# Kernel optimization log

Hardware: AMD Instinct MI355X
Metric: run time of the kernel (lower is better)

Reference implementation:

```python
import jax, jax.numpy as jnp
import numpy as np

VOCAB, EMB, H, LAYERS, B, T = 50000, 128, 128, 3, 64, 512


def _lstm_dir(x, w_ih, w_hh, b_ih, b_hh, h0, c0, reverse):
    # x: [B,T,Din]; w_ih: [4H,Din]; w_hh: [4H,H]; h0,c0: [B,H]
    xg = jnp.einsum('btd,gd->btg', x, w_ih) + b_ih + b_hh  # [B,T,4H]

    def step(carry, xg_t):
        h, c = carry
        g = xg_t + h @ w_hh.T  # [B,4H]
        i, f, gg, o = jnp.split(g, 4, axis=-1)  # torch gate order i,f,g,o
        c = jax.nn.sigmoid(f) * c + jax.nn.sigmoid(i) * jnp.tanh(gg)
        h = jax.nn.sigmoid(o) * jnp.tanh(c)
        return (h, c), h

    _, hs = jax.lax.scan(step, (h0, c0), jnp.swapaxes(xg, 0, 1), reverse=reverse)
    return jnp.swapaxes(hs, 0, 1)  # [B,T,H], aligned with input time order


def _bidir_layer(x, w_ih, w_hh, b_ih, b_hh, h0, c0):
    # stacked params: leading dim 2 = (fwd, bwd)
    fwd = _lstm_dir(x, w_ih[0], w_hh[0], b_ih[0], b_hh[0], h0[0], c0[0], False)
    bwd = _lstm_dir(x, w_ih[1], w_hh[1], b_ih[1], b_hh[1], h0[1], c0[1], True)
    return jnp.concatenate([fwd, bwd], axis=-1)  # [B,T,2H]


def setup_inputs() -> dict:
    key = jax.random.key(0)
    ks = jax.random.split(key, 20)
    s = 1.0 / np.sqrt(H)
    inp = {
        'X_batch': jax.random.randint(ks[0], (B, T), 0, VOCAB),
        'emb': jax.random.normal(ks[1], (VOCAB, EMB), jnp.float32),
        'hx': jax.random.normal(ks[2], (2 * LAYERS, B, H), jnp.float32),
        'cx': jax.random.normal(ks[3], (2 * LAYERS, B, H), jnp.float32),
        'lin_w': jax.random.uniform(ks[4], (1, 2 * H), jnp.float32, -s, s),
        'lin_b': jax.random.uniform(ks[5], (1,), jnp.float32, -s, s),
    }
    k = 6
    for l in range(LAYERS):
        din = EMB if l == 0 else 2 * H
        inp[f'w_ih_{l}'] = jax.random.uniform(ks[k], (2, 4 * H, din), jnp.float32, -s, s); k += 1
        inp[f'w_hh_{l}'] = jax.random.uniform(ks[k], (2, 4 * H, H), jnp.float32, -s, s); k += 1
        inp[f'b_ih_{l}'] = jax.random.uniform(ks[k], (2, 4 * H), jnp.float32, -s, s); k += 1
        inp[f'b_hh_{l}'] = jax.random.uniform(ks[k], (2, 4 * H), jnp.float32, -s, s); k += 1
    return inp


def reference(X_batch, emb, hx, cx, lin_w, lin_b,
              w_ih_0, w_hh_0, b_ih_0, b_hh_0,
              w_ih_1, w_hh_1, b_ih_1, b_hh_1,
              w_ih_2, w_hh_2, b_ih_2, b_hh_2):
    x = emb[X_batch]  # [B,T,EMB]
    params = [(w_ih_0, w_hh_0, b_ih_0, b_hh_0),
              (w_ih_1, w_hh_1, b_ih_1, b_hh_1),
              (w_ih_2, w_hh_2, b_ih_2, b_hh_2)]
    for l, (wi, wh, bi, bh) in enumerate(params):
        x = _bidir_layer(x, wi, wh, bi, bh, hx[2 * l:2 * l + 2], cx[2 * l:2 * l + 2])
    # linear head applied to last timestep (== output[:, -1] of full linear)
    return x[:, -1] @ lin_w.T + lin_b  # [B,1]
```

## Files before the change

### kernel.cpp

```cpp
#include <hip/hip_runtime.h>
#include <hip/hip_bf16.h>
#include <stdint.h>

#define B_    64
#define T_    512
#define EMB_  128
#define H_    128
#define G4    512
#define M_    (B_ * T_)

typedef __attribute__((ext_vector_type(8))) short     short8;
typedef __attribute__((ext_vector_type(4))) float     floatx4;
typedef __attribute__((ext_vector_type(2))) _Float16  half2v;

#define GLDS(g, l) __builtin_amdgcn_global_load_lds( \
    (__attribute__((address_space(1))) void*)(g),    \
    (__attribute__((address_space(3))) void*)(l), 16, 0, 0)

__device__ __forceinline__ unsigned short f2bf_bits(float f) {
  __hip_bfloat16 h = __float2bfloat16(f);
  return *reinterpret_cast<unsigned short*>(&h);
}
__device__ __forceinline__ float bf_bits2f(unsigned short u) {
  unsigned int x = ((unsigned int)u) << 16;
  return __uint_as_float(x);
}
__device__ __forceinline__ float sigm(float x) {
  return __fdividef(1.0f, 1.0f + __expf(-x));
}
__device__ __forceinline__ float tanh_fast(float x) {
  return 1.0f - __fdividef(2.0f, __expf(2.0f * x) + 1.0f);
}

__device__ __forceinline__ unsigned int pack_f16x2(float a, float b) {
  half2v h; h.x = (_Float16)a; h.y = (_Float16)b;
  return __builtin_bit_cast(unsigned int, h);
}
__device__ __forceinline__ half2v u2h2(unsigned int u) {
  return __builtin_bit_cast(half2v, u);
}

#if __has_builtin(__builtin_amdgcn_fdot2)
__device__ __forceinline__ float fdot2(half2v a, half2v b, float c) {
  return __builtin_amdgcn_fdot2(a, b, c, false);
}
#else
__device__ __forceinline__ float fdot2(half2v a, half2v b, float c) {
  return fmaf((float)a.x, (float)b.x, fmaf((float)a.y, (float)b.y, c));
}
#endif

__device__ __forceinline__ float pair_bfly_add(float x) {
  return x + __int_as_float(
      __builtin_amdgcn_mov_dpp(__float_as_int(x), 0xB1, 0xF, 0xF, true));
}

__device__ __forceinline__ void barrier_lds_only() {
  __builtin_amdgcn_s_waitcnt(0xC07F);
  __builtin_amdgcn_s_barrier();
}

__device__ __forceinline__ void  store_xg(float* p, float v)  { *p = v; }
__device__ __forceinline__ void  store_xg(unsigned short* p, float v) { *p = f2bf_bits(v); }
__device__ __forceinline__ float load_xg(const float* p)  { return *p; }
__device__ __forceinline__ float load_xg(const unsigned short* p) { return bf_bits2f(*p); }

__global__ void k_gather(const int* __restrict__ X, const float* __restrict__ emb,
                         unsigned short* __restrict__ x0) {
  int i = blockIdx.x * 256 + threadIdx.x;
  int row = i >> 5, c4 = i & 31;
  float4 v = ((const float4*)emb)[(size_t)X[row] * 32 + c4];
  ushort4 o;
  o.x = f2bf_bits(v.x); o.y = f2bf_bits(v.y); o.z = f2bf_bits(v.z); o.w = f2bf_bits(v.w);
  ((ushort4*)x0)[i] = o;
}

__global__ void k_prep(const float* __restrict__ w, const float* __restrict__ bi,
                       const float* __restrict__ bh, unsigned short* __restrict__ wb,
                       float* __restrict__ bias, int nw) {
  int i = blockIdx.x * blockDim.x + threadIdx.x;
  int stride = gridDim.x * blockDim.x;
  for (int k = i; k < nw; k += stride) wb[k] = f2bf_bits(w[k]);
  for (int k = i; k < 2 * G4; k += stride) bias[k] = bi[k] + bh[k];
}

__global__ void k_prep_whh(const float* __restrict__ Whh, unsigned int* __restrict__ wf) {
  int i = blockIdx.x * 256 + threadIdx.x;
  int dir = i >> 15;
  int r   = i & 0x7FFF;
  int i4  = r >> 10;
  int r2  = r & 0x3FF;
  int ts  = r2 >> 2;
  int q   = r2 & 3;
  int d   = i4 * 4 + q;
  int g   = d >> 5;
  int jj  = d & 31;
  int lane = ts & 63, w = ts >> 6;
  int p = lane & 1, ul = lane >> 1;
  int u = w * 32 + ul;
  int k = 64 * p + 2 * jj;
  const float* wr = Whh + ((size_t)dir * G4 + g * H_ + u) * H_ + k;
  wf[i] = pack_f16x2(wr[0], wr[1]);
}

template <typename XG_T>
__global__ __launch_bounds__(256, 2) void k_gemm(
    const unsigned short* __restrict__ A,
    const unsigned short* __restrict__ W,
    const float* __restrict__ bias,
    XG_T* __restrict__ xg,
    int K) {
  __shared__ unsigned short sA[128 * 32];
  __shared__ unsigned short sB[128 * 32];
  const int tid  = threadIdx.x;
  const int lane = tid & 63;
  const int wave = tid >> 6;
  const int mt = blockIdx.x, nt = blockIdx.y, dir = blockIdx.z;
  const size_t Arow0 = (size_t)mt * 128;
  const int    Ncol0 = nt * 128;
  const unsigned short* Wd = W + (size_t)dir * G4 * K;

  const int srow = tid >> 2;
  const int qlog = (tid & 3) ^ ((tid >> 4) & 3);
  auto ldsA0 = (__attribute__((address_space(3))) void*)(sA + wave * 512);
  auto ldsA1 = (__attribute__((address_space(3))) void*)(sA + 2048 + wave * 512);
  auto ldsB0 = (__attribute__((address_space(3))) void*)(sB + wave * 512);
  auto ldsB1 = (__attribute__((address_space(3))) void*)(sB + 2048 + wave * 512);

  floatx4 acc[4][4];
#pragma unroll
  for (int i = 0; i < 4; ++i)
#pragma unroll
    for (int j = 0; j < 4; ++j) acc[i][j] = (floatx4)0.0f;

  const int wrow = (wave >> 1) * 64, wcol = (wave & 1) * 64;
  const int frow = lane & 15;
  const int fq   = lane >> 4;

  for (int kt = 0; kt < K; kt += 32) {
    const unsigned short* gA0 = A  + (Arow0 + srow) * (size_t)K + kt + qlog * 8;
    const unsigned short* gB0 = Wd + (size_t)(Ncol0 + srow) * K + kt + qlog * 8;
    GLDS(gA0, ldsA0);
    GLDS(gA0 + (size_t)64 * K, ldsA1);
    GLDS(gB0, ldsB0);
    GLDS(gB0 + (size_t)64 * K, ldsB1);
    __syncthreads();

    short8 af[4], bf[4];
#pragma unroll
    for (int i = 0; i < 4; ++i) {
      int r  = wrow + 16 * i + frow;
      int rn = wcol + 16 * i + frow;
      af[i] = *(const short8*)(sA + r  * 32 + ((fq ^ ((r  >> 2) & 3)) * 8));
      bf[i] = *(const short8*)(sB + rn * 32 + ((fq ^ ((rn >> 2) & 3)) * 8));
    }
#pragma unroll
    for (int i = 0; i < 4; ++i)
#pragma unroll
      for (int j = 0; j < 4; ++j)
        acc[i][j] = __builtin_amdgcn_mfma_f32_16x16x32_bf16(af[i], bf[j], acc[i][j], 0, 0, 0);
    __syncthreads();
  }

  const int r0 = (lane >> 4) * 4;
  const int cc = lane & 15;
  XG_T* xgd = xg + (size_t)dir * M_ * G4;
#pragma unroll
  for (int j = 0; j < 4; ++j) {
    int gcol = Ncol0 + wcol + 16 * j + cc;
    float bs = bias[dir * G4 + gcol];
#pragma unroll
    for (int i = 0; i < 4; ++i) {
      size_t rowb = Arow0 + wrow + 16 * i + r0;
#pragma unroll
      for (int r = 0; r < 4; ++r)
        store_xg(&xgd[(rowb + r) * G4 + gcol], acc[i][j][r] + bs);
    }
  }
}

template <typename XG_T>
__global__ __attribute__((amdgpu_flat_work_group_size(256, 256),
                          amdgpu_waves_per_eu(1, 1))) void k_scan(
    const unsigned int* __restrict__ wf,
    const float* __restrict__ hx0,
    const float* __restrict__ cx0,
    const XG_T* __restrict__ xg,
    unsigned short* __restrict__ y)
{
  const int b   = blockIdx.x & 63;
  const int dir = blockIdx.x >> 6;
  const int tid = threadIdx.x;
  const int lane = tid & 63;
  const int wave = tid >> 6;
  const int p  = lane & 1;
  const int ul = lane >> 1;
  const int u  = wave * 32 + ul;

  __shared__ __align__(16) unsigned short h16[2][128];

  uint4 wv[32];
  const uint4* wfv = (const uint4*)wf;
#pragma unroll
  for (int i = 0; i < 32; ++i) wv[i] = wfv[(dir * 32 + i) * 256 + tid];

  float c = cx0[(size_t)dir * B_ * H_ + b * H_ + u];
  if (p == 0) {
    float h0 = hx0[(size_t)dir * B_ * H_ + b * H_ + u];
    h16[0][u] = (unsigned short)(pack_f16x2(h0, 0.0f) & 0xFFFF);
  }

  const XG_T* xgb = xg + ((size_t)dir * M_ + (size_t)b * T_) * G4;
  const intptr_t xstep = dir ? -(intptr_t)G4 : (intptr_t)G4;
  const int o0 = (2 * p) * H_ + u;
  const int o1 = o0 + H_;
  const XG_T* xrow0 = xgb + (dir ? (size_t)(T_ - 1) * G4 : 0);
  float xa0 = load_xg(xrow0 + o0), xb0 = load_xg(xrow0 + o1);
  float xa1 = load_xg(xrow0 + xstep + o0), xb1 = load_xg(xrow0 + xstep + o1);
  const XG_T* xld = xrow0 + 2 * xstep;

  unsigned short* yp = y + ((size_t)b * T_ + (dir ? T_ - 1 : 0)) * (2 * H_)
                         + dir * H_ + u;
  const intptr_t ystep = dir ? -(intptr_t)(2 * H_) : (intptr_t)(2 * H_);

  __syncthreads();

  auto dots = [&](int par, float xva, float xvb,
                  float& g0, float& g1, float& g2, float& g3) {
    const uint4* hv4 = (const uint4*)&h16[par][0];
    uint4 hq[8];
#pragma unroll
    for (int i = 0; i < 8; ++i) hq[i] = hv4[8 * p + i];
    half2v hh[32];
#pragma unroll
    for (int i = 0; i < 8; ++i) {
      hh[4 * i + 0] = u2h2(hq[i].x);
      hh[4 * i + 1] = u2h2(hq[i].y);
      hh[4 * i + 2] = u2h2(hq[i].z);
      hh[4 * i + 3] = u2h2(hq[i].w);
    }
    float A0 = 0, B0 = 0, A1 = 0, B1 = 0, A2 = 0, B2 = 0, A3 = 0, B3 = 0;
#pragma unroll
    for (int j = 0; j < 16; ++j) {
      int d0 = j, d1 = j + 16;
      A0 = fdot2(u2h2(((const unsigned int*)&wv[(0 * 32 + d0) >> 2])[(0 * 32 + d0) & 3]), hh[d0], A0);
      A1 = fdot2(u2h2(((const unsigned int*)&wv[(1 * 32 + d0) >> 2])[(1 * 32 + d0) & 3]), hh[d0], A1);
      A2 = fdot2(u2h2(((const unsigned int*)&wv[(2 * 32 + d0) >> 2])[(2 * 32 + d0) & 3]), hh[d0], A2);
      A3 = fdot2(u2h2(((const unsigned int*)&wv[(3 * 32 + d0) >> 2])[(3 * 32 + d0) & 3]), hh[d0], A3);
      B0 = fdot2(u2h2(((const unsigned int*)&wv[(0 * 32 + d1) >> 2])[(0 * 32 + d1) & 3]), hh[d1], B0);
      B1 = fdot2(u2h2(((const unsigned int*)&wv[(1 * 32 + d1) >> 2])[(1 * 32 + d1) & 3]), hh[d1], B1);
      B2 = fdot2(u2h2(((const unsigned int*)&wv[(2 * 32 + d1) >> 2])[(2 * 32 + d1) & 3]), hh[d1], B2);
      B3 = fdot2(u2h2(((const unsigned int*)&wv[(3 * 32 + d1) >> 2])[(3 * 32 + d1) & 3]), hh[d1], B3);
    }
    g0 = A0 + B0; g1 = A1 + B1; g2 = A2 + B2; g3 = A3 + B3;
    g0 += (p == 0) ? xva : 0.0f;
    g1 += (p == 0) ? xvb : 0.0f;
    g2 += (p == 1) ? xva : 0.0f;
    g3 += (p == 1) ? xvb : 0.0f;
  };

  auto finish = [&](int par, float g0, float g1, float g2, float g3) {
    g0 = pair_bfly_add(g0);
    g1 = pair_bfly_add(g1);
    g2 = pair_bfly_add(g2);
    g3 = pair_bfly_add(g3);
    float iv = sigm(g0), fv = sigm(g1), gv = tanh_fast(g2), ov = sigm(g3);
    c = fmaf(fv, c, iv * gv);
    float h = ov * tanh_fast(c);
    if (p == 0) {
      h16[par ^ 1][u] = (unsigned short)(pack_f16x2(h, 0.0f) & 0xFFFF);
      *yp = f2bf_bits(h);
    }
    yp += ystep;
    barrier_lds_only();
  };

  for (int t = 0; t < T_; t += 2) {
    {
      float va = xa0, vb = xb0;
      if (t + 2 < T_) { xa0 = load_xg(xld + o0); xb0 = load_xg(xld + o1); }
      else            { xa0 = 0.0f; xb0 = 0.0f; }
      xld += xstep;
      float a0, a1, a2, a3;
      dots(0, va, vb, a0, a1, a2, a3);
      finish(0, a0, a1, a2, a3);
    }
    {
      float va = xa1, vb = xb1;
      if (t + 3 < T_) { xa1 = load_xg(xld + o0); xb1 = load_xg(xld + o1); }
      else            { xa1 = 0.0f; xb1 = 0.0f; }
      xld += xstep;
      float a0, a1, a2, a3;
      dots(1, va, vb, a0, a1, a2, a3);
      finish(1, a0, a1, a2, a3);
    }
  }
}

__global__ void k_head(const unsigned short* __restrict__ y2, const float* __restrict__ lw,
                       const float* __restrict__ lb, float* __restrict__ out) {
  int b = blockIdx.x, l = threadIdx.x;
  const unsigned short* row = y2 + ((size_t)b * T_ + (T_ - 1)) * (2 * H_);
  float s = 0;
#pragma unroll
  for (int k = 0; k < 4; ++k) s += bf_bits2f(row[l + 64 * k]) * lw[l + 64 * k];
#pragma unroll
  for (int off = 32; off > 0; off >>= 1) s += __shfl_down(s, off);
  if (l == 0) out[b] = s + lb[0];
}

template <typename XG_T>
static inline void run_layers(const unsigned int* const* wfs,
                              const unsigned short* x0,
                              unsigned short* y0, unsigned short* y1, unsigned short* y2,
                              const unsigned short* wb0, const unsigned short* wb1,
                              const unsigned short* wb2,
                              const float* bias0, const float* bias1, const float* bias2,
                              const float* hx, const float* cx,
                              XG_T* xg, hipStream_t stream) {
  dim3 gg(M_ / 128, G4 / 128, 2);
  k_gemm<XG_T><<<gg, 256, 0, stream>>>(x0, wb0, bias0, xg, EMB_);
  k_scan<XG_T><<<128, 256, 0, stream>>>(wfs[0], hx, cx, xg, y0);
  k_gemm<XG_T><<<gg, 256, 0, stream>>>(y0, wb1, bias1, xg, 2 * H_);
  k_scan<XG_T><<<128, 256, 0, stream>>>(wfs[1], hx + 2 * B_ * H_, cx + 2 * B_ * H_, xg, y1);
  k_gemm<XG_T><<<gg, 256, 0, stream>>>(y1, wb2, bias2, xg, 2 * H_);
  k_scan<XG_T><<<128, 256, 0, stream>>>(wfs[2], hx + 4 * B_ * H_, cx + 4 * B_ * H_, xg, y2);
}

extern "C" void kernel_launch(void* const* d_in, const int* in_sizes, int n_in,
                              void* d_out, int out_size, void* d_ws, size_t ws_size,
                              hipStream_t stream) {
  const int*   X   = (const int*)d_in[0];
  const float* emb = (const float*)d_in[1];
  const float* hx  = (const float*)d_in[2];
  const float* cx  = (const float*)d_in[3];
  const float* lw  = (const float*)d_in[4];
  const float* lb  = (const float*)d_in[5];
  const float* w_ih[3] = {(const float*)d_in[6],  (const float*)d_in[10], (const float*)d_in[14]};
  const float* w_hh[3] = {(const float*)d_in[7],  (const float*)d_in[11], (const float*)d_in[15]};
  const float* b_ih[3] = {(const float*)d_in[8],  (const float*)d_in[12], (const float*)d_in[16]};
  const float* b_hh[3] = {(const float*)d_in[9],  (const float*)d_in[13], (const float*)d_in[17]};
  float* out = (float*)d_out;

  char* ws = (char*)d_ws;
  size_t off = 0;
  auto carve = [&](size_t bytes) {
    char* p = ws + off;
    off = (off + bytes + 255) & ~(size_t)255;
    return p;
  };
  unsigned short* x0  = (unsigned short*)carve((size_t)M_ * EMB_ * 2);
  unsigned short* y0  = (unsigned short*)carve((size_t)M_ * 2 * H_ * 2);
  unsigned short* y1  = (unsigned short*)carve((size_t)M_ * 2 * H_ * 2);
  unsigned short* y2  = (unsigned short*)carve((size_t)M_ * 2 * H_ * 2);
  unsigned short* wb0 = (unsigned short*)carve((size_t)2 * G4 * EMB_ * 2);
  unsigned short* wb1 = (unsigned short*)carve((size_t)2 * G4 * 2 * H_ * 2);
  unsigned short* wb2 = (unsigned short*)carve((size_t)2 * G4 * 2 * H_ * 2);
  float* bias0 = (float*)carve(2 * G4 * 4);
  float* bias1 = (float*)carve(2 * G4 * 4);
  float* bias2 = (float*)carve(2 * G4 * 4);
  unsigned int* wf0 = (unsigned int*)carve((size_t)65536 * 4);
  unsigned int* wf1 = (unsigned int*)carve((size_t)65536 * 4);
  unsigned int* wf2 = (unsigned int*)carve((size_t)65536 * 4);
  const size_t xg_f32_bytes = (size_t)2 * M_ * G4 * 4;
  const bool use_f32 = (off + xg_f32_bytes) <= ws_size;
  void* xg = carve(use_f32 ? xg_f32_bytes : xg_f32_bytes / 2);

  k_prep<<<256, 256, 0, stream>>>(w_ih[0], b_ih[0], b_hh[0], wb0, bias0, 2 * G4 * EMB_);
  k_prep<<<256, 256, 0, stream>>>(w_ih[1], b_ih[1], b_hh[1], wb1, bias1, 2 * G4 * 2 * H_);
  k_prep<<<256, 256, 0, stream>>>(w_ih[2], b_ih[2], b_hh[2], wb2, bias2, 2 * G4 * 2 * H_);
  k_prep_whh<<<256, 256, 0, stream>>>(w_hh[0], wf0);
  k_prep_whh<<<256, 256, 0, stream>>>(w_hh[1], wf1);
  k_prep_whh<<<256, 256, 0, stream>>>(w_hh[2], wf2);
  k_gather<<<(M_ * 32) / 256, 256, 0, stream>>>(X, emb, x0);

  const unsigned int* wfs[3] = {wf0, wf1, wf2};
  if (use_f32)
    run_layers<float>(wfs, x0, y0, y1, y2, wb0, wb1, wb2, bias0, bias1, bias2,
                      hx, cx, (float*)xg, stream);
  else
    run_layers<unsigned short>(wfs, x0, y0, y1, y2, wb0, wb1, wb2, bias0, bias1, bias2,
                               hx, cx, (unsigned short*)xg, stream);

  k_head<<<64, 64, 0, stream>>>(y2, lw, lb, out);
}
```

Baseline: 1.114 ms.

## Split each LSTM hidden unit across four lanes in 512-thread scan blocks

The recurrent scan kernel now uses 512 threads per block, with four lanes per hidden unit instead of two. Each lane holds 64 packed fp16 weight registers instead of 128 and runs a shorter fdot2 chain per step. The partial sums are combined with a two-step DPP quad reduction. The weight pre-pack kernel is reordered to match this layout, and the prefetch bounds checks are dropped. The aim is to cut the serial latency of each timestep, at the cost of an extra shuffle stage, a barrier across twice as many waves, and harmless over-reads past the sequence end.

```diff
diff --git a/kernel.cpp b/kernel.cpp
--- a/kernel.cpp
+++ b/kernel.cpp
@@ -50,9 +50,12 @@
 }
 #endif
 
-__device__ __forceinline__ float pair_bfly_add(float x) {
-  return x + __int_as_float(
+__device__ __forceinline__ float quad_sum(float x) {
+  x += __int_as_float(
       __builtin_amdgcn_mov_dpp(__float_as_int(x), 0xB1, 0xF, 0xF, true));
+  x += __int_as_float(
+      __builtin_amdgcn_mov_dpp(__float_as_int(x), 0x4E, 0xF, 0xF, true));
+  return x;
 }
 
 __device__ __forceinline__ void barrier_lds_only() {
@@ -86,20 +89,17 @@
 
 __global__ void k_prep_whh(const float* __restrict__ Whh, unsigned int* __restrict__ wf) {
   int i = blockIdx.x * 256 + threadIdx.x;
-  int dir = i >> 15;
-  int r   = i & 0x7FFF;
-  int i4  = r >> 10;
-  int r2  = r & 0x3FF;
-  int ts  = r2 >> 2;
-  int q   = r2 & 3;
-  int d   = i4 * 4 + q;
-  int g   = d >> 5;
-  int jj  = d & 31;
-  int lane = ts & 63, w = ts >> 6;
-  int p = lane & 1, ul = lane >> 1;
-  int u = w * 32 + ul;
-  int k = 64 * p + 2 * jj;
-  const float* wr = Whh + ((size_t)dir * G4 + g * H_ + u) * H_ + k;
+  int dir   = i >> 15;
+  int r     = i & 0x7FFF;
+  int plane = r >> 9;
+  int ts    = r & 511;
+  int g = plane >> 4;
+  int j = plane & 15;
+  int l = ts & 63, w = ts >> 6;
+  int p2 = l & 3, ul = l >> 2;
+  int u  = w * 16 + ul;
+  int k0 = 32 * p2 + 2 * j;
+  const float* wr = Whh + ((size_t)dir * G4 + g * H_ + u) * H_ + k0;
   wf[i] = pack_f16x2(wr[0], wr[1]);
 }
 
@@ -180,8 +180,8 @@
 }
 
 template <typename XG_T>
-__global__ __attribute__((amdgpu_flat_work_group_size(256, 256),
-                          amdgpu_waves_per_eu(1, 1))) void k_scan(
+__global__ __attribute__((amdgpu_flat_work_group_size(512, 512),
+                          amdgpu_waves_per_eu(2, 2))) void k_scan(
     const unsigned int* __restrict__ wf,
     const float* __restrict__ hx0,
     const float* __restrict__ cx0,
@@ -193,30 +193,28 @@
   const int tid = threadIdx.x;
   const int lane = tid & 63;
   const int wave = tid >> 6;
-  const int p  = lane & 1;
-  const int ul = lane >> 1;
-  const int u  = wave * 32 + ul;
+  const int p2 = lane & 3;
+  const int ul = lane >> 2;
+  const int u  = wave * 16 + ul;
 
   __shared__ __align__(16) unsigned short h16[2][128];
 
-  uint4 wv[32];
-  const uint4* wfv = (const uint4*)wf;
-#pragma unroll
-  for (int i = 0; i < 32; ++i) wv[i] = wfv[(dir * 32 + i) * 256 + tid];
+  unsigned int wvs[64];
+#pragma unroll
+  for (int i = 0; i < 64; ++i) wvs[i] = wf[((dir * 64 + i) << 9) + tid];
 
   float c = cx0[(size_t)dir * B_ * H_ + b * H_ + u];
-  if (p == 0) {
+  if (p2 == 0) {
     float h0 = hx0[(size_t)dir * B_ * H_ + b * H_ + u];
     h16[0][u] = (unsigned short)(pack_f16x2(h0, 0.0f) & 0xFFFF);
   }
 
   const XG_T* xgb = xg + ((size_t)dir * M_ + (size_t)b * T_) * G4;
   const intptr_t xstep = dir ? -(intptr_t)G4 : (intptr_t)G4;
-  const int o0 = (2 * p) * H_ + u;
-  const int o1 = o0 + H_;
+  const int o0 = p2 * H_ + u;
   const XG_T* xrow0 = xgb + (dir ? (size_t)(T_ - 1) * G4 : 0);
-  float xa0 = load_xg(xrow0 + o0), xb0 = load_xg(xrow0 + o1);
-  float xa1 = load_xg(xrow0 + xstep + o0), xb1 = load_xg(xrow0 + xstep + o1);
+  float xa0 = load_xg(xrow0 + o0);
+  float xa1 = load_xg(xrow0 + xstep + o0);
   const XG_T* xld = xrow0 + 2 * xstep;
 
   unsigned short* yp = y + ((size_t)b * T_ + (dir ? T_ - 1 : 0)) * (2 * H_)
@@ -225,49 +223,41 @@
 
   __syncthreads();
 
-  auto dots = [&](int par, float xva, float xvb,
-                  float& g0, float& g1, float& g2, float& g3) {
-    const uint4* hv4 = (const uint4*)&h16[par][0];
-    uint4 hq[8];
-#pragma unroll
-    for (int i = 0; i < 8; ++i) hq[i] = hv4[8 * p + i];
-    half2v hh[32];
-#pragma unroll
-    for (int i = 0; i < 8; ++i) {
-      hh[4 * i + 0] = u2h2(hq[i].x);
-      hh[4 * i + 1] = u2h2(hq[i].y);
-      hh[4 * i + 2] = u2h2(hq[i].z);
-      hh[4 * i + 3] = u2h2(hq[i].w);
-    }
-    float A0 = 0, B0 = 0, A1 = 0, B1 = 0, A2 = 0, B2 = 0, A3 = 0, B3 = 0;
-#pragma unroll
-    for (int j = 0; j < 16; ++j) {
-      int d0 = j, d1 = j + 16;
-      A0 = fdot2(u2h2(((const unsigned int*)&wv[(0 * 32 + d0) >> 2])[(0 * 32 + d0) & 3]), hh[d0], A0);
-      A1 = fdot2(u2h2(((const unsigned int*)&wv[(1 * 32 + d0) >> 2])[(1 * 32 + d0) & 3]), hh[d0], A1);
-      A2 = fdot2(u2h2(((const unsigned int*)&wv[(2 * 32 + d0) >> 2])[(2 * 32 + d0) & 3]), hh[d0], A2);
-      A3 = fdot2(u2h2(((const unsigned int*)&wv[(3 * 32 + d0) >> 2])[(3 * 32 + d0) & 3]), hh[d0], A3);
-      B0 = fdot2(u2h2(((const unsigned int*)&wv[(0 * 32 + d1) >> 2])[(0 * 32 + d1) & 3]), hh[d1], B0);
-      B1 = fdot2(u2h2(((const unsigned int*)&wv[(1 * 32 + d1) >> 2])[(1 * 32 + d1) & 3]), hh[d1], B1);
-      B2 = fdot2(u2h2(((const unsigned int*)&wv[(2 * 32 + d1) >> 2])[(2 * 32 + d1) & 3]), hh[d1], B2);
-      B3 = fdot2(u2h2(((const unsigned int*)&wv[(3 * 32 + d1) >> 2])[(3 * 32 + d1) & 3]), hh[d1], B3);
-    }
-    g0 = A0 + B0; g1 = A1 + B1; g2 = A2 + B2; g3 = A3 + B3;
-    g0 += (p == 0) ? xva : 0.0f;
-    g1 += (p == 0) ? xvb : 0.0f;
-    g2 += (p == 1) ? xva : 0.0f;
-    g3 += (p == 1) ? xvb : 0.0f;
-  };
-
-  auto finish = [&](int par, float g0, float g1, float g2, float g3) {
-    g0 = pair_bfly_add(g0);
-    g1 = pair_bfly_add(g1);
-    g2 = pair_bfly_add(g2);
-    g3 = pair_bfly_add(g3);
+  auto step = [&](int par, float xv) {
+    const char* hb = (const char*)&h16[par][0] + 64 * p2;
+    uint4 hq[4];
+#pragma unroll
+    for (int i = 0; i < 4; ++i) hq[i] = *(const uint4*)(hb + 16 * i);
+    unsigned int hhd[16];
+#pragma unroll
+    for (int i = 0; i < 4; ++i) {
+      hhd[4 * i + 0] = hq[i].x; hhd[4 * i + 1] = hq[i].y;
+      hhd[4 * i + 2] = hq[i].z; hhd[4 * i + 3] = hq[i].w;
+    }
+    float A0 = (p2 == 0) ? xv : 0.0f, B0 = 0;
+    float A1 = (p2 == 1) ? xv : 0.0f, B1 = 0;
+    float A2 = (p2 == 2) ? xv : 0.0f, B2 = 0;
+    float A3 = (p2 == 3) ? xv : 0.0f, B3 = 0;
+#pragma unroll
+    for (int j = 0; j < 8; ++j) {
+      int j1 = j + 8;
+      A0 = fdot2(u2h2(wvs[0 * 16 + j]),  u2h2(hhd[j]),  A0);
+      A1 = fdot2(u2h2(wvs[1 * 16 + j]),  u2h2(hhd[j]),  A1);
+      A2 = fdot2(u2h2(wvs[2 * 16 + j]),  u2h2(hhd[j]),  A2);
+      A3 = fdot2(u2h2(wvs[3 * 16 + j]),  u2h2(hhd[j]),  A3);
+      B0 = fdot2(u2h2(wvs[0 * 16 + j1]), u2h2(hhd[j1]), B0);
+      B1 = fdot2(u2h2(wvs[1 * 16 + j1]), u2h2(hhd[j1]), B1);
+      B2 = fdot2(u2h2(wvs[2 * 16 + j1]), u2h2(hhd[j1]), B2);
+      B3 = fdot2(u2h2(wvs[3 * 16 + j1]), u2h2(hhd[j1]), B3);
+    }
+    float g0 = quad_sum(A0 + B0);
+    float g1 = quad_sum(A1 + B1);
+    float g2 = quad_sum(A2 + B2);
+    float g3 = quad_sum(A3 + B3);
     float iv = sigm(g0), fv = sigm(g1), gv = tanh_fast(g2), ov = sigm(g3);
     c = fmaf(fv, c, iv * gv);
     float h = ov * tanh_fast(c);
-    if (p == 0) {
+    if (p2 == 0) {
       h16[par ^ 1][u] = (unsigned short)(pack_f16x2(h, 0.0f) & 0xFFFF);
       *yp = f2bf_bits(h);
     }
@@ -277,22 +267,16 @@
 
   for (int t = 0; t < T_; t += 2) {
     {
-      float va = xa0, vb = xb0;
-      if (t + 2 < T_) { xa0 = load_xg(xld + o0); xb0 = load_xg(xld + o1); }
-      else            { xa0 = 0.0f; xb0 = 0.0f; }
+      float xv = xa0;
+      xa0 = load_xg(xld + o0);
       xld += xstep;
-      float a0, a1, a2, a3;
-      dots(0, va, vb, a0, a1, a2, a3);
-      finish(0, a0, a1, a2, a3);
+      step(0, xv);
     }
     {
-      float va = xa1, vb = xb1;
-      if (t + 3 < T_) { xa1 = load_xg(xld + o0); xb1 = load_xg(xld + o1); }
-      else            { xa1 = 0.0f; xb1 = 0.0f; }
+      float xv = xa1;
+      xa1 = load_xg(xld + o0);
       xld += xstep;
-      float a0, a1, a2, a3;
-      dots(1, va, vb, a0, a1, a2, a3);
-      finish(1, a0, a1, a2, a3);
+      step(1, xv);
     }
   }
 }
@@ -320,11 +304,11 @@
                               XG_T* xg, hipStream_t stream) {
   dim3 gg(M_ / 128, G4 / 128, 2);
   k_gemm<XG_T><<<gg, 256, 0, stream>>>(x0, wb0, bias0, xg, EMB_);
-  k_scan<XG_T><<<128, 256, 0, stream>>>(wfs[0], hx, cx, xg, y0);
+  k_scan<XG_T><<<128, 512, 0, stream>>>(wfs[0], hx, cx, xg, y0);
   k_gemm<XG_T><<<gg, 256, 0, stream>>>(y0, wb1, bias1, xg, 2 * H_);
-  k_scan<XG_T><<<128, 256, 0, stream>>>(wfs[1], hx + 2 * B_ * H_, cx + 2 * B_ * H_, xg, y1);
+  k_scan<XG_T><<<128, 512, 0, stream>>>(wfs[1], hx + 2 * B_ * H_, cx + 2 * B_ * H_, xg, y1);
   k_gemm<XG_T><<<gg, 256, 0, stream>>>(y1, wb2, bias2, xg, 2 * H_);
-  k_scan<XG_T><<<128, 256, 0, stream>>>(wfs[2], hx + 4 * B_ * H_, cx + 4 * B_ * H_, xg, y2);
+  k_scan<XG_T><<<128, 512, 0, stream>>>(wfs[2], hx + 4 * B_ * H_, cx + 4 * B_ * H_, xg, y2);
 }
 
 extern "C" void kernel_launch(void* const* d_in, const int* in_sizes, int n_in,
```

Result: slower. 1.370 ms (+22.9%).
